# Kernel optimization log

Measured on AMD Instinct MI355X. Metric: run time of the kernel, lower is better.

## Reference

```python
import jax, jax.numpy as jnp
import numpy as np

HEADS = 16
DIM_HEAD = 64
DIM = 1024
INNER = HEADS * DIM_HEAD  # 1024


def setup_inputs() -> dict:
    key = jax.random.key(0)
    ks = jax.random.split(key, 8)
    B, N, M = 4, 2048, 2048
    x = jax.random.normal(ks[0], (B, N, DIM), dtype=jnp.float32)
    context = jax.random.normal(ks[1], (B, M, DIM), dtype=jnp.float32)
    x_mask = (jax.random.uniform(ks[2], (B, N)) > 0.1).astype(jnp.float32)
    context_mask = (jax.random.uniform(ks[3], (B, M)) > 0.1).astype(jnp.float32)
    s = 0.02
    Wq = jax.random.normal(ks[4], (DIM, INNER), dtype=jnp.float32) * s
    Wkv = jax.random.normal(ks[5], (DIM, 2 * INNER), dtype=jnp.float32) * s
    Wo = jax.random.normal(ks[6], (INNER, DIM), dtype=jnp.float32) * s
    bo = jnp.zeros((DIM,), dtype=jnp.float32)
    return {"x": x, "context": context, "x_mask": x_mask,
            "context_mask": context_mask, "Wq": Wq, "Wkv": Wkv, "Wo": Wo, "bo": bo}


def _split_heads(t):
    b, n, _ = t.shape
    return t.reshape(b, n, HEADS, DIM_HEAD).transpose(0, 2, 1, 3)  # b h n d


def reference(x, context, x_mask, context_mask, Wq, Wkv, Wo, bo):
    scale = DIM_HEAD ** -0.5
    q = _split_heads(x @ Wq)                       # b h n d
    kv = context @ Wkv
    k = _split_heads(kv[..., :INNER])              # b h m d
    v = _split_heads(kv[..., INNER:])              # b h m d
    dots = jnp.einsum('bhnd,bhmd->bhnm', q, k) * scale
    # attn_bias = 1 - x_mask ⊗ context_mask; masked where isclose(attn_bias, 1)
    prod = x_mask[:, None, :, None] * context_mask[:, None, None, :]  # b 1 n m
    masked = jnp.isclose(1.0 - prod, 1.0)          # b 1 n m, broadcast over heads
    dots = jnp.where(masked, -jnp.inf, dots)       # b h n m
    # rows with no valid key: zero the whole row before softmax
    valid = jnp.any(~masked, axis=-1, keepdims=True)  # b 1 n 1
    dots = jnp.where(valid, dots, 0.0)
    attn = jax.nn.softmax(dots, axis=-1)
    attn = jnp.where(valid, attn, 0.0)
    out = jnp.einsum('bhnm,bhmd->bhnd', attn, v)
    b, h, n, d = out.shape
    out = out.transpose(0, 2, 1, 3).reshape(b, n, h * d)
    return out @ Wo + bo
```

## Files before the change

kernel.cpp:

```cpp
#include <hip/hip_runtime.h>

#define DEVI __device__ __forceinline__

typedef __attribute__((ext_vector_type(4))) float f32x4;
typedef __attribute__((ext_vector_type(8))) _Float16 f16x8;
typedef __attribute__((ext_vector_type(2))) _Float16 f16x2;
typedef __attribute__((ext_vector_type(4))) unsigned u32x4;

#if __has_builtin(__builtin_amdgcn_exp2f)
#define EXP2F __builtin_amdgcn_exp2f
#else
#define EXP2F exp2f
#endif

DEVI ushort f2h(float f) {
  _Float16 h = (_Float16)f;
  return __builtin_bit_cast(ushort, h);
}

DEVI unsigned pkrtz(float a, float b) {
  return __builtin_bit_cast(unsigned, __builtin_amdgcn_cvt_pkrtz(a, b));
}

DEVI void gload_lds16(const void* g, void* l) {
  typedef const unsigned int GlobU __attribute__((address_space(1)));
  typedef unsigned int LdsU __attribute__((address_space(3)));
  __builtin_amdgcn_global_load_lds((GlobU*)g, (LdsU*)l, 16, 0, 0);
}

__global__ __launch_bounds__(256) void cast_f16_kernel(
    const float4* __restrict__ x, const float4* __restrict__ ctx,
    ushort4* __restrict__ xo, ushort4* __restrict__ co) {
  int i = blockIdx.x * 256 + threadIdx.x;
  const float4* src;
  ushort4* dst;
  int j;
  if (i < 2097152) { src = x; dst = xo; j = i; }
  else             { src = ctx; dst = co; j = i - 2097152; }
  float4 v = src[j];
  ushort4 o;
  o.x = f2h(v.x); o.y = f2h(v.y); o.z = f2h(v.z); o.w = f2h(v.w);
  dst[j] = o;
}

__global__ __launch_bounds__(256) void transpose_cast_kernel(
    const float* __restrict__ Wq, const float* __restrict__ Wkv,
    const float* __restrict__ Wo, ushort* __restrict__ WqT,
    ushort* __restrict__ WkvT, ushort* __restrict__ WoT) {
  __shared__ ushort tile[64][65];
  int bx = blockIdx.x;
  const float* in; ushort* out; int C, cb;
  if (bx < 16)      { in = Wq;  out = WqT;  C = 1024; cb = bx * 64; }
  else if (bx < 48) { in = Wkv; out = WkvT; C = 2048; cb = (bx - 16) * 64; }
  else              { in = Wo;  out = WoT;  C = 1024; cb = (bx - 48) * 64; }
  const int R = 1024;
  int rb = blockIdx.y * 64;
  int t = threadIdx.x;
  int c4 = (t & 15) * 4, r0 = t >> 4;
#pragma unroll
  for (int i = 0; i < 4; i++) {
    int r = r0 + i * 16;
    float4 v = *(const float4*)(in + (size_t)(rb + r) * C + cb + c4);
    tile[r][c4 + 0] = f2h(v.x);
    tile[r][c4 + 1] = f2h(v.y);
    tile[r][c4 + 2] = f2h(v.z);
    tile[r][c4 + 3] = f2h(v.w);
  }
  __syncthreads();
#pragma unroll
  for (int i = 0; i < 4; i++) {
    int rr = r0 + i * 16;
    ushort4 o;
    o.x = tile[c4 + 0][rr]; o.y = tile[c4 + 1][rr];
    o.z = tile[c4 + 2][rr]; o.w = tile[c4 + 3][rr];
    *(ushort4*)(out + (size_t)(cb + rr) * R + rb + c4) = o;
  }
}

DEVI void gemm_stage(const ushort* __restrict__ A, const ushort* __restrict__ Bt,
                     int K, int rowbase, int colbase, int tid, int wave,
                     ushort* AsC, ushort* BsC, int kk) {
#pragma unroll
  for (int i = 0; i < 2; i++) {
    int f = i * 256 + tid;
    int r = f >> 2;
    int c = (f & 3) ^ (r & 3);
    gload_lds16(A + (size_t)(rowbase + r) * K + (kk + c * 8),
                (char*)AsC + (size_t)(i * 256 + wave * 64) * 16);
    gload_lds16(Bt + (size_t)(colbase + r) * K + (kk + c * 8),
                (char*)BsC + (size_t)(i * 256 + wave * 64) * 16);
  }
}

DEVI void gemm_core(const ushort* __restrict__ A, const ushort* __restrict__ Bt,
                    const int K, int rowbase, int colbase, int tid,
                    ushort* As, ushort* Bs, f32x4 acc[4][4]) {
  const int lane = tid & 63, wave = tid >> 6;
  const int quad = lane >> 4, ln = lane & 15;
  const int wrow = (wave >> 1) * 64, wcol = (wave & 1) * 64;

  gemm_stage(A, Bt, K, rowbase, colbase, tid, wave, As, Bs, 0);
  gemm_stage(A, Bt, K, rowbase, colbase, tid, wave, As + 4096, Bs + 4096, 32);

  for (int k0 = 0; k0 < K; k0 += 32) {
    const int cur = (k0 >> 5) & 1;
    ushort* AsC = As + cur * 4096;
    ushort* BsC = Bs + cur * 4096;

    if (k0 + 32 < K) asm volatile("s_waitcnt vmcnt(4)" ::: "memory");
    else             asm volatile("s_waitcnt vmcnt(0)" ::: "memory");
    asm volatile("s_barrier" ::: "memory");

    f16x8 a[4], b[4];
#pragma unroll
    for (int mt = 0; mt < 4; mt++) {
      int r = wrow + mt * 16 + ln;
      a[mt] = *(const f16x8*)(AsC + ((size_t)r * 4 + (quad ^ (r & 3))) * 8);
    }
#pragma unroll
    for (int nt = 0; nt < 4; nt++) {
      int r = wcol + nt * 16 + ln;
      b[nt] = *(const f16x8*)(BsC + ((size_t)r * 4 + (quad ^ (r & 3))) * 8);
    }
#pragma unroll
    for (int mt = 0; mt < 4; mt++)
#pragma unroll
      for (int nt = 0; nt < 4; nt++)
        acc[mt][nt] = __builtin_amdgcn_mfma_f32_16x16x32_f16(a[mt], b[nt], acc[mt][nt], 0, 0, 0);

    asm volatile("s_barrier" ::: "memory");
    if (k0 + 64 < K)
      gemm_stage(A, Bt, K, rowbase, colbase, tid, wave, AsC, BsC, k0 + 64);
  }
}

__global__ __launch_bounds__(256, 3) void qkv_gemm(
    const ushort* __restrict__ xb, const ushort* __restrict__ cb,
    const ushort* __restrict__ WqT, const ushort* __restrict__ WkvT,
    ushort* __restrict__ Qo, ushort* __restrict__ Ko, ushort* __restrict__ Vo) {
  __shared__ ushort As[2 * 128 * 32];
  __shared__ ushort Bs[2 * 128 * 32];
  const int tid = threadIdx.x;
  const int lane = tid & 63, wave = tid >> 6;
  const int quad = lane >> 4, ln = lane & 15;
  const int cy = blockIdx.y;
  const bool isQ = cy < 8;
  const int colbase = (isQ ? cy : cy - 8) * 128;
  const int rowbase = blockIdx.x * 128;
  const int wrow = (wave >> 1) * 64, wcol = (wave & 1) * 64;
  f32x4 acc[4][4] = {};
  gemm_core(isQ ? xb : cb, isQ ? WqT : WkvT, 1024, rowbase, colbase, tid, As, Bs, acc);

  if (isQ) {
    const float qs = 0.18033688011112042f;
#pragma unroll
    for (int nt = 0; nt < 4; nt++) {
      int col = colbase + wcol + nt * 16 + ln;
      int h = col >> 6, d = col & 63;
#pragma unroll
      for (int mt = 0; mt < 4; mt++) {
        int row = rowbase + wrow + mt * 16 + quad * 4;
        int bb = row >> 11, n = row & 2047;
        uint2 pv;
        pv.x = pkrtz(acc[mt][nt][0] * qs, acc[mt][nt][1] * qs);
        pv.y = pkrtz(acc[mt][nt][2] * qs, acc[mt][nt][3] * qs);
        *(uint2*)(Qo + (((size_t)bb * 16 + h) * 64 + d) * 2048 + n) = pv;
      }
    }
  } else {
    bool isK = (colbase < 1024);
#pragma unroll
    for (int nt = 0; nt < 4; nt++) {
      int col = colbase + wcol + nt * 16 + ln;
#pragma unroll
      for (int mt = 0; mt < 4; mt++) {
        int row = rowbase + wrow + mt * 16 + quad * 4;
        int bb = row >> 11, m = row & 2047;
        if (isK) {
          int h = col >> 6, d = col & 63;
#pragma unroll
          for (int r = 0; r < 4; r++)
            Ko[(((size_t)bb * 16 + h) * 2048 + (m + r)) * 64 + d] = f2h(acc[mt][nt][r]);
        } else {
          int c2 = col - 1024;
          int h = c2 >> 6, d = c2 & 63;
          uint2 pv;
          pv.x = pkrtz(acc[mt][nt][0], acc[mt][nt][1]);
          pv.y = pkrtz(acc[mt][nt][2], acc[mt][nt][3]);
          *(uint2*)(Vo + (((size_t)bb * 16 + h) * 64 + d) * 2048 + m) = pv;
        }
      }
    }
  }
}

__global__ __launch_bounds__(256, 3) void out_gemm(
    const ushort* __restrict__ A, const ushort* __restrict__ Bt,
    float* __restrict__ C, const float* __restrict__ bias) {
  __shared__ ushort As[2 * 128 * 32];
  __shared__ ushort Bs[2 * 128 * 32];
  const int tid = threadIdx.x;
  const int lane = tid & 63, wave = tid >> 6;
  const int quad = lane >> 4, ln = lane & 15;
  const int colbase = blockIdx.y * 128, rowbase = blockIdx.x * 128;
  const int wrow = (wave >> 1) * 64, wcol = (wave & 1) * 64;
  f32x4 acc[4][4] = {};
  gemm_core(A, Bt, 1024, rowbase, colbase, tid, As, Bs, acc);
#pragma unroll
  for (int nt = 0; nt < 4; nt++) {
    int col = colbase + wcol + nt * 16 + ln;
    float bv = bias[col];
#pragma unroll
    for (int mt = 0; mt < 4; mt++) {
      int row = rowbase + wrow + mt * 16 + quad * 4;
#pragma unroll
      for (int r = 0; r < 4; r++)
        C[(size_t)(row + r) * 1024 + col] = acc[mt][nt][r] + bv;
    }
  }
}

__global__ __launch_bounds__(256, 2) void attn_kernel(
    const ushort* __restrict__ QT, const ushort* __restrict__ K,
    const ushort* __restrict__ VT, const float* __restrict__ xmask,
    const float* __restrict__ cmask, ushort* __restrict__ O) {
  __shared__ ushort Ks[3][64 * 64];
  __shared__ ushort Vs[3][64 * 64];
  __shared__ float CMB[2048];
  const int tid = threadIdx.x, lane = tid & 63, wave = tid >> 6;
  const int quad = lane >> 4, ln = lane & 15;
  const int bid = blockIdx.x;
  const int qb = bid >> 6, bh6 = bid & 63, h = bh6 & 15, b = bh6 >> 4;
  const size_t bh = (size_t)b * 16 + h;
  const ushort* QTbh = QT + bh * (64 * 2048);
  const ushort* Kbh = K + bh * (2048 * 64);
  const ushort* Vbh = VT + bh * (64 * 2048);
  const int q0 = qb * 256 + wave * 64;

#pragma unroll
  for (int i = 0; i < 2; i++) {
    float4 c0 = *(const float4*)(cmask + b * 2048 + tid * 8 + i * 4);
    float4 b0;
    b0.x = fmaf(c0.x, 3.0e4f, -3.0e4f); b0.y = fmaf(c0.y, 3.0e4f, -3.0e4f);
    b0.z = fmaf(c0.z, 3.0e4f, -3.0e4f); b0.w = fmaf(c0.w, 3.0e4f, -3.0e4f);
    *(float4*)(CMB + tid * 8 + i * 4) = b0;
  }

  f16x8 qf[4][2];
#pragma unroll
  for (int qt = 0; qt < 4; qt++)
#pragma unroll
    for (int kc = 0; kc < 2; kc++) {
      int q = q0 + qt * 16 + ln;
#pragma unroll
      for (int j = 0; j < 8; j++)
        qf[qt][kc][j] = __builtin_bit_cast(_Float16,
            (unsigned short)QTbh[(size_t)(kc * 32 + quad * 8 + j) * 2048 + q]);
    }

  float xm[4];
#pragma unroll
  for (int qt = 0; qt < 4; qt++) xm[qt] = xmask[b * 2048 + q0 + qt * 16 + ln];

  __syncthreads();

  auto STAGE = [&](int t, int buf) {
#pragma unroll
    for (int i = 0; i < 2; i++) {
      int f = i * 256 + tid;
      int r = f >> 3;
      int c = (f & 7) ^ (r & 7);
      int rp = (r & 32) | ((r & 12) << 1) | ((r & 16) >> 2) | (r & 3);
      gload_lds16(Kbh + (size_t)(t * 64 + rp) * 64 + c * 8, (char*)Ks[buf] + (size_t)f * 16);
      gload_lds16(Vbh + (size_t)r * 2048 + (t * 64 + c * 8), (char*)Vs[buf] + (size_t)f * 16);
    }
  };

  STAGE(0, 0);
  STAGE(1, 1);

  f16x8 onesf;
#pragma unroll
  for (int j = 0; j < 8; j++) onesf[j] = (_Float16)1.0f;

  f32x4 o[4][4] = {};
  f32x4 lsum[4] = {};

  int cur = 0;
  for (int kb = 0; kb < 32; kb++) {
    const int m0 = kb * 64;
    const ushort* KsC = Ks[cur];
    const ushort* VsC = Vs[cur];

    if (kb < 31) asm volatile("s_waitcnt vmcnt(4)" ::: "memory");
    else         asm volatile("s_waitcnt vmcnt(0)" ::: "memory");
    asm volatile("s_barrier" ::: "memory");

    f32x4 bias4[4];
#pragma unroll
    for (int kt = 0; kt < 4; kt++)
      bias4[kt] = *(const f32x4*)(CMB + m0 + (kt >> 1) * 32 + quad * 8 + (kt & 1) * 4);

    f32x4 s[4][4];
#pragma unroll
    for (int kt = 0; kt < 4; kt++)
#pragma unroll
      for (int qt = 0; qt < 4; qt++) s[kt][qt] = bias4[kt];
    __builtin_amdgcn_s_setprio(1);
#pragma unroll
    for (int kc = 0; kc < 2; kc++) {
#pragma unroll
      for (int kt = 0; kt < 4; kt++) {
        int r = kt * 16 + ln;
        f16x8 ka = *(const f16x8*)(KsC + ((size_t)r * 8 + ((kc * 4 + quad) ^ (r & 7))) * 8);
#pragma unroll
        for (int qt = 0; qt < 4; qt++)
          s[kt][qt] = __builtin_amdgcn_mfma_f32_16x16x32_f16(ka, qf[qt][kc], s[kt][qt], 0, 0, 0);
      }
    }
    __builtin_amdgcn_s_setprio(0);

#pragma unroll
    for (int kc = 0; kc < 2; kc++) {
      f16x8 pf[4];
#pragma unroll
      for (int qt = 0; qt < 4; qt++) {
        f32x4 sA = s[kc * 2 + 0][qt];
        f32x4 sB = s[kc * 2 + 1][qt];
        u32x4 u;
        u[0] = pkrtz(EXP2F(sA[0]), EXP2F(sA[1]));
        u[1] = pkrtz(EXP2F(sA[2]), EXP2F(sA[3]));
        u[2] = pkrtz(EXP2F(sB[0]), EXP2F(sB[1]));
        u[3] = pkrtz(EXP2F(sB[2]), EXP2F(sB[3]));
        pf[qt] = __builtin_bit_cast(f16x8, u);
      }
      __builtin_amdgcn_s_setprio(1);
#pragma unroll
      for (int qt = 0; qt < 4; qt++)
        lsum[qt] = __builtin_amdgcn_mfma_f32_16x16x32_f16(onesf, pf[qt], lsum[qt], 0, 0, 0);
#pragma unroll
      for (int dt = 0; dt < 4; dt++) {
        int r = dt * 16 + ln;
        f16x8 va = *(const f16x8*)(VsC + ((size_t)r * 8 + ((kc * 4 + quad) ^ (r & 7))) * 8);
#pragma unroll
        for (int qt = 0; qt < 4; qt++)
          o[dt][qt] = __builtin_amdgcn_mfma_f32_16x16x32_f16(va, pf[qt], o[dt][qt], 0, 0, 0);
      }
      __builtin_amdgcn_s_setprio(0);
    }

    if (kb < 30) {
      int nxt = cur - 1; if (nxt < 0) nxt = 2;
      STAGE(kb + 2, nxt);
    }
    cur = cur + 1; if (cur == 3) cur = 0;
  }

#pragma unroll
  for (int qt = 0; qt < 4; qt++) {
    float l = lsum[qt][0];
    float inv = (xm[qt] != 0.f && l > 0.f) ? (1.f / l) : 0.f;
    int n = q0 + qt * 16 + ln;
    ushort* ob = O + ((size_t)(b * 2048 + n) * 16 + h) * 64;
#pragma unroll
    for (int dt = 0; dt < 4; dt++) {
      uint2 pv;
      pv.x = pkrtz(o[dt][qt][0] * inv, o[dt][qt][1] * inv);
      pv.y = pkrtz(o[dt][qt][2] * inv, o[dt][qt][3] * inv);
      *(uint2*)(ob + dt * 16 + quad * 4) = pv;
    }
  }
}

extern "C" void kernel_launch(void* const* d_in, const int* in_sizes, int n_in,
                              void* d_out, int out_size, void* d_ws, size_t ws_size,
                              hipStream_t stream) {
  const float* x   = (const float*)d_in[0];
  const float* ctx = (const float*)d_in[1];
  const float* xm  = (const float*)d_in[2];
  const float* cm  = (const float*)d_in[3];
  const float* Wq  = (const float*)d_in[4];
  const float* Wkv = (const float*)d_in[5];
  const float* Wo  = (const float*)d_in[6];
  const float* bo  = (const float*)d_in[7];

  char* ws = (char*)d_ws;
  const size_t MB = 1024 * 1024;
  ushort* xb   = (ushort*)(ws + 0);
  ushort* cb   = (ushort*)(ws + 16 * MB);
  ushort* WqT  = (ushort*)(ws + 32 * MB);
  ushort* WkvT = (ushort*)(ws + 34 * MB);
  ushort* WoT  = (ushort*)(ws + 38 * MB);
  ushort* QTb  = (ushort*)(ws + 40 * MB);
  ushort* Kb   = (ushort*)(ws + 56 * MB);
  ushort* VTb  = (ushort*)(ws + 72 * MB);
  ushort* Ob   = xb;

  cast_f16_kernel<<<16384, 256, 0, stream>>>((const float4*)x, (const float4*)ctx,
                                             (ushort4*)xb, (ushort4*)cb);
  transpose_cast_kernel<<<dim3(64, 16), 256, 0, stream>>>(Wq, Wkv, Wo, WqT, WkvT, WoT);
  qkv_gemm<<<dim3(64, 24), 256, 0, stream>>>(xb, cb, WqT, WkvT, QTb, Kb, VTb);
  attn_kernel<<<512, 256, 0, stream>>>(QTb, Kb, VTb, xm, cm, Ob);
  out_gemm<<<dim3(64, 8), 256, 0, stream>>>(Ob, WoT, (float*)d_out, bo);
}
```

Before: 303.1 us.

## Triple-buffer GEMM LDS, drop trailing barrier, fuse prep kernels

The GEMM k-loop moves from two to three LDS buffers, so the prefetch for step k+2 writes a buffer nobody is reading. That lets the second barrier per iteration be removed. MFMA sections are raised in wave priority with s_setprio. The fp16 cast and weight transpose kernels are merged into a single launch to save one kernel launch. LDS use per block rises to 48KB, which may limit occupancy.

```diff
diff --git a/kernel.cpp b/kernel.cpp
--- a/kernel.cpp
+++ b/kernel.cpp
@@ -28,34 +28,36 @@
   __builtin_amdgcn_global_load_lds((GlobU*)g, (LdsU*)l, 16, 0, 0);
 }
 
-__global__ __launch_bounds__(256) void cast_f16_kernel(
+__global__ __launch_bounds__(256) void prep_kernel(
     const float4* __restrict__ x, const float4* __restrict__ ctx,
-    ushort4* __restrict__ xo, ushort4* __restrict__ co) {
-  int i = blockIdx.x * 256 + threadIdx.x;
-  const float4* src;
-  ushort4* dst;
-  int j;
-  if (i < 2097152) { src = x; dst = xo; j = i; }
-  else             { src = ctx; dst = co; j = i - 2097152; }
-  float4 v = src[j];
-  ushort4 o;
-  o.x = f2h(v.x); o.y = f2h(v.y); o.z = f2h(v.z); o.w = f2h(v.w);
-  dst[j] = o;
-}
-
-__global__ __launch_bounds__(256) void transpose_cast_kernel(
+    ushort4* __restrict__ xo, ushort4* __restrict__ co,
     const float* __restrict__ Wq, const float* __restrict__ Wkv,
     const float* __restrict__ Wo, ushort* __restrict__ WqT,
     ushort* __restrict__ WkvT, ushort* __restrict__ WoT) {
   __shared__ ushort tile[64][65];
-  int bx = blockIdx.x;
+  const int bid = blockIdx.x;
+  const int t = threadIdx.x;
+  if (bid < 16384) {
+    int i = bid * 256 + t;
+    const float4* src;
+    ushort4* dst;
+    int j;
+    if (i < 2097152) { src = x; dst = xo; j = i; }
+    else             { src = ctx; dst = co; j = i - 2097152; }
+    float4 v = src[j];
+    ushort4 o;
+    o.x = f2h(v.x); o.y = f2h(v.y); o.z = f2h(v.z); o.w = f2h(v.w);
+    dst[j] = o;
+    return;
+  }
+  int bx2 = bid - 16384;
+  int bx = bx2 & 63;
+  int rb = (bx2 >> 6) * 64;
   const float* in; ushort* out; int C, cb;
   if (bx < 16)      { in = Wq;  out = WqT;  C = 1024; cb = bx * 64; }
   else if (bx < 48) { in = Wkv; out = WkvT; C = 2048; cb = (bx - 16) * 64; }
   else              { in = Wo;  out = WoT;  C = 1024; cb = (bx - 48) * 64; }
   const int R = 1024;
-  int rb = blockIdx.y * 64;
-  int t = threadIdx.x;
   int c4 = (t & 15) * 4, r0 = t >> 4;
 #pragma unroll
   for (int i = 0; i < 4; i++) {
@@ -102,8 +104,8 @@
   gemm_stage(A, Bt, K, rowbase, colbase, tid, wave, As, Bs, 0);
   gemm_stage(A, Bt, K, rowbase, colbase, tid, wave, As + 4096, Bs + 4096, 32);
 
+  int cur = 0;
   for (int k0 = 0; k0 < K; k0 += 32) {
-    const int cur = (k0 >> 5) & 1;
     ushort* AsC = As + cur * 4096;
     ushort* BsC = Bs + cur * 4096;
 
@@ -122,15 +124,19 @@
       int r = wcol + nt * 16 + ln;
       b[nt] = *(const f16x8*)(BsC + ((size_t)r * 4 + (quad ^ (r & 3))) * 8);
     }
+    __builtin_amdgcn_s_setprio(1);
 #pragma unroll
     for (int mt = 0; mt < 4; mt++)
 #pragma unroll
       for (int nt = 0; nt < 4; nt++)
         acc[mt][nt] = __builtin_amdgcn_mfma_f32_16x16x32_f16(a[mt], b[nt], acc[mt][nt], 0, 0, 0);
-
-    asm volatile("s_barrier" ::: "memory");
-    if (k0 + 64 < K)
-      gemm_stage(A, Bt, K, rowbase, colbase, tid, wave, AsC, BsC, k0 + 64);
+    __builtin_amdgcn_s_setprio(0);
+
+    if (k0 + 64 < K) {
+      int nxt = cur - 1; if (nxt < 0) nxt = 2;
+      gemm_stage(A, Bt, K, rowbase, colbase, tid, wave, As + nxt * 4096, Bs + nxt * 4096, k0 + 64);
+    }
+    cur = cur + 1; if (cur == 3) cur = 0;
   }
 }
 
@@ -138,8 +144,8 @@
     const ushort* __restrict__ xb, const ushort* __restrict__ cb,
     const ushort* __restrict__ WqT, const ushort* __restrict__ WkvT,
     ushort* __restrict__ Qo, ushort* __restrict__ Ko, ushort* __restrict__ Vo) {
-  __shared__ ushort As[2 * 128 * 32];
-  __shared__ ushort Bs[2 * 128 * 32];
+  __shared__ ushort As[3 * 128 * 32];
+  __shared__ ushort Bs[3 * 128 * 32];
   const int tid = threadIdx.x;
   const int lane = tid & 63, wave = tid >> 6;
   const int quad = lane >> 4, ln = lane & 15;
@@ -197,8 +203,8 @@
 __global__ __launch_bounds__(256, 3) void out_gemm(
     const ushort* __restrict__ A, const ushort* __restrict__ Bt,
     float* __restrict__ C, const float* __restrict__ bias) {
-  __shared__ ushort As[2 * 128 * 32];
-  __shared__ ushort Bs[2 * 128 * 32];
+  __shared__ ushort As[3 * 128 * 32];
+  __shared__ ushort Bs[3 * 128 * 32];
   const int tid = threadIdx.x;
   const int lane = tid & 63, wave = tid >> 6;
   const int quad = lane >> 4, ln = lane & 15;
@@ -396,9 +402,9 @@
   ushort* VTb  = (ushort*)(ws + 72 * MB);
   ushort* Ob   = xb;
 
-  cast_f16_kernel<<<16384, 256, 0, stream>>>((const float4*)x, (const float4*)ctx,
-                                             (ushort4*)xb, (ushort4*)cb);
-  transpose_cast_kernel<<<dim3(64, 16), 256, 0, stream>>>(Wq, Wkv, Wo, WqT, WkvT, WoT);
+  prep_kernel<<<17408, 256, 0, stream>>>((const float4*)x, (const float4*)ctx,
+                                         (ushort4*)xb, (ushort4*)cb,
+                                         Wq, Wkv, Wo, WqT, WkvT, WoT);
   qkv_gemm<<<dim3(64, 24), 256, 0, stream>>>(xb, cb, WqT, WkvT, QTb, Kb, VTb);
   attn_kernel<<<512, 256, 0, stream>>>(QTb, Kb, VTb, xm, cm, Ob);
   out_gemm<<<dim3(64, 8), 256, 0, stream>>>(Ob, WoT, (float*)d_out, bo);
```

After: 303.3 us. No clear change (+0.1%).
